# Kernel optimization log

Measured on AMD Instinct MI355X. Metric: run time of the kernel, lower is better.

## Reference

```python
import jax, jax.numpy as jnp
import numpy as np

B, D, HID = 16384, 1024, 4096
HALF = D // 2


def setup_inputs() -> dict:
    key = jax.random.key(0)
    ks = jax.random.split(key, 9)
    sc_in = 1.0 / np.sqrt(HALF)
    sc_h = 1.0 / np.sqrt(HID)
    return {
        "z": jax.random.normal(ks[0], (B, D), dtype=jnp.float32),
        "W1s": jax.random.uniform(ks[1], (HALF, HID), jnp.float32, -sc_in, sc_in),
        "b1s": jax.random.uniform(ks[2], (HID,), jnp.float32, -sc_in, sc_in),
        "W2s": jax.random.uniform(ks[3], (HID, HALF), jnp.float32, -sc_h, sc_h),
        "b2s": jax.random.uniform(ks[4], (HALF,), jnp.float32, -sc_h, sc_h),
        "W1t": jax.random.uniform(ks[5], (HALF, HID), jnp.float32, -sc_in, sc_in),
        "b1t": jax.random.uniform(ks[6], (HID,), jnp.float32, -sc_in, sc_in),
        "W2t": jax.random.uniform(ks[7], (HID, HALF), jnp.float32, -sc_h, sc_h),
        "b2t": jax.random.uniform(ks[8], (HALF,), jnp.float32, -sc_h, sc_h),
    }


def reference(z, W1s, b1s, W2s, b2s, W1t, b1t, W2t, b2t):
    # mask_even=True: a = even-indexed features, b = odd-indexed features
    a = z[:, 0::2]  # [B, HALF]
    b = z[:, 1::2]  # [B, HALF]
    # two-layer MLPs for s and t (cond=None -> inp = a)
    s = jnp.maximum(a @ W1s + b1s, 0.0) @ W2s + b2s  # [B, HALF]
    t = jnp.maximum(a @ W1t + b1t, 0.0) @ W2t + b2t  # [B, HALF]
    b_out = b * jnp.exp(s) + t
    logdet = s.sum(axis=1)  # [B]
    # scatter back: a -> even slots, b_out -> odd slots (interleave)
    z_out = jnp.stack([a, b_out], axis=-1).reshape(z.shape)
    return z_out, logdet
```

## Files before the change

### kernel.cpp

```cpp
#include <hip/hip_runtime.h>
#include <hip/hip_bf16.h>
#include <cstdint>
#include <cstddef>

#define BROWS  16384
#define DDIM   1024
#define HID_N  4096
#define HALF_K 512
#define LDH    8192

typedef __attribute__((ext_vector_type(8))) short s8v;
typedef __attribute__((ext_vector_type(4))) float f4v;

__device__ __forceinline__ void gload16(const void* g, void* l) {
  __builtin_amdgcn_global_load_lds(
      (const __attribute__((address_space(1))) unsigned int*)g,
      (__attribute__((address_space(3))) unsigned int*)l, 16, 0, 0);
}
#define BAR()   asm volatile("s_barrier" ::: "memory")
#define BARS()  asm volatile("s_waitcnt lgkmcnt(0)\n\ts_barrier" ::: "memory")
#define SCHED0() __builtin_amdgcn_sched_barrier(0)

template <int N> __device__ __forceinline__ void vmw() {
  if constexpr (N == 0)      asm volatile("s_waitcnt vmcnt(0)" ::: "memory");
  else if constexpr (N == 4) asm volatile("s_waitcnt vmcnt(4)" ::: "memory");
  else if constexpr (N == 8) asm volatile("s_waitcnt vmcnt(8)" ::: "memory");
}

__global__ __launch_bounds__(256) void cast_a_kernel(const float* __restrict__ z,
                                                     __hip_bfloat16* __restrict__ a16) {
  const int idx = blockIdx.x * 256 + threadIdx.x;
  const int m  = idx >> 6;
  const int kb = idx & 63;
  const float4* zp = (const float4*)(z + (size_t)m * DDIM + (size_t)kb * 16);
  alignas(16) __hip_bfloat16 t[8];
#pragma unroll
  for (int i = 0; i < 4; ++i) {
    float4 v = zp[i];
    t[2 * i]     = __float2bfloat16(v.x);
    t[2 * i + 1] = __float2bfloat16(v.z);
  }
  *(s8v*)(a16 + (size_t)m * HALF_K + kb * 8) = *(const s8v*)t;
}

__global__ __launch_bounds__(256) void transpose_cast_kernel(const float* __restrict__ W,
                                                             __hip_bfloat16* __restrict__ WT,
                                                             int K, int N) {
  __shared__ float tile[32][33];
  const int n0 = blockIdx.x * 32, k0 = blockIdx.y * 32;
  const int tx = threadIdx.x & 31;
  const int ty = threadIdx.x >> 5;
#pragma unroll
  for (int i = 0; i < 32; i += 8)
    tile[ty + i][tx] = W[(size_t)(k0 + ty + i) * N + n0 + tx];
  __syncthreads();
#pragma unroll
  for (int i = 0; i < 32; i += 8)
    WT[(size_t)(n0 + ty + i) * K + k0 + tx] = __float2bfloat16(tile[tx][ty + i]);
}

__global__ __launch_bounds__(512, 2)
void gemm1_kernel(const __hip_bfloat16* __restrict__ A,
                  const __hip_bfloat16* __restrict__ BT,
                  const float* __restrict__ b1s, const float* __restrict__ b1t,
                  __hip_bfloat16* __restrict__ Hout) {
  __shared__ alignas(16) char smem[131072];
  constexpr int NT = HALF_K / 64;

  const int nwg = gridDim.x;
  const int orig = blockIdx.x;
  const int vid = (orig & 7) * (nwg >> 3) + (orig >> 3);
  const int bx = vid >> 5, by = vid & 31;
  const int m0 = bx * 256, n0 = by * 256;

  const int tid = threadIdx.x;
  const int trow = tid >> 3;
  const int scol = ((tid & 7) * 16) ^ ((trow & 7) << 4);

  const int lane = tid & 63, wid = tid >> 6;
  const int wr = wid >> 2, wc = wid & 3;
  const int lr = lane & 15, lk = lane >> 4;
  const int xo = (lr & 7) << 4;

  int aoff[4][2], boff[2][2];
#pragma unroll
  for (int j = 0; j < 4; ++j)
#pragma unroll
    for (int kk = 0; kk < 2; ++kk)
      aoff[j][kk] = (j * 32 + wr * 16 + lr) * 128 + ((kk * 64 + lk * 16) ^ xo);
#pragma unroll
  for (int nn = 0; nn < 2; ++nn)
#pragma unroll
    for (int kk = 0; kk < 2; ++kk)
      boff[nn][kk] = (nn * 64 + wc * 16 + lr) * 128 + ((kk * 64 + lk * 16) ^ xo);

  f4v acc[8][4] = {};

  auto stage_A = [&](int h, int T) {
#pragma unroll
    for (int l = 0; l < 2; ++l)
      gload16((const char*)A + (size_t)(m0 + h * 128 + l * 64 + trow) * (HALF_K * 2) + (size_t)T * 128 + scol,
              smem + (T & 1) * 65536 + h * 16384 + l * 8192 + tid * 16);
  };
  auto stage_B = [&](int h, int T) {
#pragma unroll
    for (int l = 0; l < 2; ++l)
      gload16((const char*)BT + (size_t)(n0 + h * 128 + l * 64 + trow) * (HALF_K * 2) + (size_t)T * 128 + scol,
              smem + (T & 1) * 65536 + 32768 + h * 16384 + l * 8192 + tid * 16);
  };

  stage_A(0, 0); stage_B(0, 0); stage_A(1, 0); stage_B(1, 0);
  stage_A(0, 1); stage_B(0, 1);
  vmw<4>();
  BAR();

  for (int T = 0; T < NT; ++T) {
    const char* bufp = smem + (T & 1) * 65536;
    s8v af[4][2], b0r[2][2], b1r[2][2];

#pragma unroll
    for (int j = 0; j < 4; ++j) {
      af[j][0] = *(const s8v*)(bufp + aoff[j][0]);
      af[j][1] = *(const s8v*)(bufp + aoff[j][1]);
    }
#pragma unroll
    for (int nn = 0; nn < 2; ++nn) {
      b0r[nn][0] = *(const s8v*)(bufp + 32768 + boff[nn][0]);
      b0r[nn][1] = *(const s8v*)(bufp + 32768 + boff[nn][1]);
    }
    if (T + 1 < NT) stage_B(1, T + 1);
    BAR(); SCHED0();
    __builtin_amdgcn_s_setprio(1);
#pragma unroll
    for (int j = 0; j < 4; ++j)
#pragma unroll
      for (int nn = 0; nn < 2; ++nn)
#pragma unroll
        for (int kk = 0; kk < 2; ++kk)
          acc[j][nn] = __builtin_amdgcn_mfma_f32_16x16x32_bf16(af[j][kk], b0r[nn][kk], acc[j][nn], 0, 0, 0);
    __builtin_amdgcn_s_setprio(0);
    BAR();

#pragma unroll
    for (int nn = 0; nn < 2; ++nn) {
      b1r[nn][0] = *(const s8v*)(bufp + 49152 + boff[nn][0]);
      b1r[nn][1] = *(const s8v*)(bufp + 49152 + boff[nn][1]);
    }
    if (T + 1 < NT) stage_A(1, T + 1);
    BAR(); SCHED0();
    __builtin_amdgcn_s_setprio(1);
#pragma unroll
    for (int j = 0; j < 4; ++j)
#pragma unroll
      for (int nn = 0; nn < 2; ++nn)
#pragma unroll
        for (int kk = 0; kk < 2; ++kk)
          acc[j][2 + nn] = __builtin_amdgcn_mfma_f32_16x16x32_bf16(af[j][kk], b1r[nn][kk], acc[j][2 + nn], 0, 0, 0);
    __builtin_amdgcn_s_setprio(0);
    BAR();

#pragma unroll
    for (int j = 0; j < 4; ++j) {
      af[j][0] = *(const s8v*)(bufp + 16384 + aoff[j][0]);
      af[j][1] = *(const s8v*)(bufp + 16384 + aoff[j][1]);
    }
    if (T + 2 < NT) stage_A(0, T + 2);
    BAR(); SCHED0();
    __builtin_amdgcn_s_setprio(1);
#pragma unroll
    for (int j = 0; j < 4; ++j)
#pragma unroll
      for (int nn = 0; nn < 2; ++nn)
#pragma unroll
        for (int kk = 0; kk < 2; ++kk)
          acc[4 + j][nn] = __builtin_amdgcn_mfma_f32_16x16x32_bf16(af[j][kk], b0r[nn][kk], acc[4 + j][nn], 0, 0, 0);
    __builtin_amdgcn_s_setprio(0);
    BAR();

    if (T + 2 < NT) stage_B(0, T + 2);
    SCHED0();
    __builtin_amdgcn_s_setprio(1);
#pragma unroll
    for (int j = 0; j < 4; ++j)
#pragma unroll
      for (int nn = 0; nn < 2; ++nn)
#pragma unroll
        for (int kk = 0; kk < 2; ++kk)
          acc[4 + j][2 + nn] = __builtin_amdgcn_mfma_f32_16x16x32_bf16(af[j][kk], b1r[nn][kk], acc[4 + j][2 + nn], 0, 0, 0);
    __builtin_amdgcn_s_setprio(0);
    if (T + 2 >= NT) vmw<0>(); else vmw<4>();
    BAR();
  }

  const float* bp = (n0 < HID_N) ? b1s : b1t;
  const int cb0 = n0 & (HID_N - 1);
  float bv[4];
#pragma unroll
  for (int ni = 0; ni < 4; ++ni) bv[ni] = bp[cb0 + ni * 64 + wc * 16 + lr];
  const int rbase = wr * 16 + lk * 4;

#pragma unroll
  for (int mi = 0; mi < 8; ++mi) {
    BARS();
#pragma unroll
    for (int ni = 0; ni < 4; ++ni) {
      const int cb = (ni * 64 + wc * 16 + lr) * 2;
#pragma unroll
      for (int r = 0; r < 4; ++r) {
        const int row = rbase + r;
        float v = fmaxf(acc[mi][ni][r] + bv[ni], 0.0f);
        *(__hip_bfloat16*)(smem + row * 512 + (cb ^ ((row & 7) << 4))) = __float2bfloat16(v);
      }
    }
    BARS();
#pragma unroll
    for (int i = 0; i < 2; ++i) {
      const int bo = tid * 32 + i * 16;
      const int row = bo >> 9, cb = bo & 511;
      s8v v = *(const s8v*)(smem + row * 512 + (cb ^ ((row & 7) << 4)));
      *(s8v*)((char*)Hout + ((size_t)(m0 + mi * 32 + row) * LDH + n0) * 2 + cb) = v;
    }
  }
}

__global__ __launch_bounds__(512, 2)
void gemm2_kernel(const __hip_bfloat16* __restrict__ H,
                  const __hip_bfloat16* __restrict__ BsT,
                  const __hip_bfloat16* __restrict__ BtT,
                  const float* __restrict__ b2s, const float* __restrict__ b2t,
                  const float* __restrict__ zin, float* __restrict__ zout,
                  float* __restrict__ gpart) {
  __shared__ alignas(16) char smem[131072];
  constexpr int NT = HID_N / 64;

  const int nwg = gridDim.x;
  const int orig = blockIdx.x;
  const int vid = (orig & 7) * (nwg >> 3) + (orig >> 3);
  const int rb = vid >> 2, by = vid & 3;
  const int m0 = rb * 128, n0c = by * 128;

  const int tid = threadIdx.x;
  const int trow = tid >> 3;
  const int scol = ((tid & 7) * 16) ^ ((trow & 7) << 4);

  const int lane = tid & 63, wid = tid >> 6;
  const int wr = wid >> 2, wc = wid & 3;
  const int lr = lane & 15, lk = lane >> 4;
  const int xo = (lr & 7) << 4;

  int aoff[4][2], boff[2][2];
#pragma unroll
  for (int j = 0; j < 4; ++j)
#pragma unroll
    for (int kk = 0; kk < 2; ++kk)
      aoff[j][kk] = (j * 32 + wr * 16 + lr) * 128 + ((kk * 64 + lk * 16) ^ xo);
#pragma unroll
  for (int nn = 0; nn < 2; ++nn)
#pragma unroll
    for (int kk = 0; kk < 2; ++kk)
      boff[nn][kk] = (nn * 64 + wc * 16 + lr) * 128 + ((kk * 64 + lk * 16) ^ xo);

  f4v as[4][2] = {}, at[4][2] = {};

  auto stage_As = [&](int T) {
#pragma unroll
    for (int l = 0; l < 2; ++l)
      gload16((const char*)H + (size_t)(m0 + l * 64 + trow) * (LDH * 2) + (size_t)T * 128 + scol,
              smem + (T & 1) * 65536 + l * 8192 + tid * 16);
  };
  auto stage_At = [&](int T) {
#pragma unroll
    for (int l = 0; l < 2; ++l)
      gload16((const char*)H + (size_t)(m0 + l * 64 + trow) * (LDH * 2) + 8192 + (size_t)T * 128 + scol,
              smem + (T & 1) * 65536 + 16384 + l * 8192 + tid * 16);
  };
  auto stage_Bs = [&](int T) {
#pragma unroll
    for (int l = 0; l < 2; ++l)
      gload16((const char*)BsT + (size_t)(n0c + l * 64 + trow) * (HID_N * 2) + (size_t)T * 128 + scol,
              smem + (T & 1) * 65536 + 32768 + l * 8192 + tid * 16);
  };
  auto stage_Bt = [&](int T) {
#pragma unroll
    for (int l = 0; l < 2; ++l)
      gload16((const char*)BtT + (size_t)(n0c + l * 64 + trow) * (HID_N * 2) + (size_t)T * 128 + scol,
              smem + (T & 1) * 65536 + 49152 + l * 8192 + tid * 16);
  };

  stage_As(0); stage_Bs(0); stage_At(0); stage_Bt(0); stage_As(1); stage_Bs(1);
  vmw<8>();
  BAR();

  for (int T = 0; T < NT; ++T) {
    const char* bufp = smem + (T & 1) * 65536;
    s8v af[4][2], bfr[2][2];

#pragma unroll
    for (int j = 0; j < 4; ++j) {
      af[j][0] = *(const s8v*)(bufp + aoff[j][0]);
      af[j][1] = *(const s8v*)(bufp + aoff[j][1]);
    }
#pragma unroll
    for (int nn = 0; nn < 2; ++nn) {
      bfr[nn][0] = *(const s8v*)(bufp + 32768 + boff[nn][0]);
      bfr[nn][1] = *(const s8v*)(bufp + 32768 + boff[nn][1]);
    }
    if (T + 1 < NT) { stage_At(T + 1); stage_Bt(T + 1); }
    BAR(); SCHED0();
    __builtin_amdgcn_s_setprio(1);
#pragma unroll
    for (int j = 0; j < 4; ++j)
#pragma unroll
      for (int nn = 0; nn < 2; ++nn)
#pragma unroll
        for (int kk = 0; kk < 2; ++kk)
          as[j][nn] = __builtin_amdgcn_mfma_f32_16x16x32_bf16(af[j][kk], bfr[nn][kk], as[j][nn], 0, 0, 0);
    __builtin_amdgcn_s_setprio(0);
    if (T + 1 >= NT) vmw<0>(); else vmw<8>();
    BAR();

#pragma unroll
    for (int j = 0; j < 4; ++j) {
      af[j][0] = *(const s8v*)(bufp + 16384 + aoff[j][0]);
      af[j][1] = *(const s8v*)(bufp + 16384 + aoff[j][1]);
    }
#pragma unroll
    for (int nn = 0; nn < 2; ++nn) {
      bfr[nn][0] = *(const s8v*)(bufp + 49152 + boff[nn][0]);
      bfr[nn][1] = *(const s8v*)(bufp + 49152 + boff[nn][1]);
    }
    if (T + 2 < NT) { stage_As(T + 2); stage_Bs(T + 2); }
    BAR(); SCHED0();
    __builtin_amdgcn_s_setprio(1);
#pragma unroll
    for (int j = 0; j < 4; ++j)
#pragma unroll
      for (int nn = 0; nn < 2; ++nn)
#pragma unroll
        for (int kk = 0; kk < 2; ++kk)
          at[j][nn] = __builtin_amdgcn_mfma_f32_16x16x32_bf16(af[j][kk], bfr[nn][kk], at[j][nn], 0, 0, 0);
    __builtin_amdgcn_s_setprio(0);
    if (T + 2 >= NT) vmw<0>(); else vmw<8>();
    BAR();
  }

  float bvs[2], bvt[2];
#pragma unroll
  for (int ni = 0; ni < 2; ++ni) {
    const int c = n0c + ni * 64 + wc * 16 + lr;
    bvs[ni] = b2s[c];
    bvt[ni] = b2t[c];
  }
  float pl[4][4] = {};
#pragma unroll
  for (int mi = 0; mi < 4; ++mi) {
#pragma unroll
    for (int ni = 0; ni < 2; ++ni) {
      const int cg = n0c + ni * 64 + wc * 16 + lr;
#pragma unroll
      for (int r = 0; r < 4; ++r) {
        const int rr = m0 + mi * 32 + wr * 16 + lk * 4 + r;
        const float sv = as[mi][ni][r] + bvs[ni];
        const float tv = at[mi][ni][r] + bvt[ni];
        pl[mi][r] += sv;
        const size_t base = (size_t)rr * DDIM + 2 * cg;
        float2 zv = *(const float2*)(zin + base);
        float2 o;
        o.x = zv.x;
        o.y = zv.y * __expf(sv) + tv;
        *(float2*)(zout + base) = o;
      }
    }
  }
#pragma unroll
  for (int m = 1; m < 16; m <<= 1)
#pragma unroll
    for (int mi = 0; mi < 4; ++mi)
#pragma unroll
      for (int r = 0; r < 4; ++r)
        pl[mi][r] += __shfl_xor(pl[mi][r], m, 64);

  float (*ldp)[4] = (float (*)[4])smem;
  BARS();
  if (lr == 0) {
#pragma unroll
    for (int mi = 0; mi < 4; ++mi)
#pragma unroll
      for (int r = 0; r < 4; ++r)
        ldp[mi * 32 + wr * 16 + lk * 4 + r][wc] = pl[mi][r];
  }
  BARS();
  if (tid < 128) {
    float v = ldp[tid][0] + ldp[tid][1] + ldp[tid][2] + ldp[tid][3];
    gpart[(size_t)(m0 + tid) * 4 + by] = v;
  }
}

__global__ __launch_bounds__(256) void ld_reduce_kernel(const float* __restrict__ gpart,
                                                        float* __restrict__ ld) {
  const int r = blockIdx.x * 256 + threadIdx.x;
  float4 v = ((const float4*)gpart)[r];
  ld[r] = v.x + v.y + v.z + v.w;
}

extern "C" void kernel_launch(void* const* d_in, const int* in_sizes, int n_in,
                              void* d_out, int out_size, void* d_ws, size_t ws_size,
                              hipStream_t stream) {
  const float* z   = (const float*)d_in[0];
  const float* W1s = (const float*)d_in[1];
  const float* b1s = (const float*)d_in[2];
  const float* W2s = (const float*)d_in[3];
  const float* b2s = (const float*)d_in[4];
  const float* W1t = (const float*)d_in[5];
  const float* b1t = (const float*)d_in[6];
  const float* W2t = (const float*)d_in[7];
  const float* b2t = (const float*)d_in[8];
  float* zout = (float*)d_out;
  float* ld   = zout + (size_t)BROWS * DDIM;

  char* ws = (char*)d_ws;
  __hip_bfloat16* a16    = (__hip_bfloat16*)ws;
  __hip_bfloat16* w1catT = (__hip_bfloat16*)(ws + 16777216);
  __hip_bfloat16* w2sT   = (__hip_bfloat16*)(ws + 25165824);
  __hip_bfloat16* w2tT   = (__hip_bfloat16*)(ws + 29360128);
  float*          gpart  = (float*)(ws + 33554432);
  char*           hbase  = ws + 33816576;

  int CH = 2048;
  for (int c = 8192; c >= 2048; c >>= 1) {
    if (33816576ull + (size_t)c * 16384ull <= ws_size) { CH = c; break; }
  }
  __hip_bfloat16* H = (__hip_bfloat16*)hbase;

  cast_a_kernel<<<BROWS * (HALF_K / 8) / 256, 256, 0, stream>>>(z, a16);
  transpose_cast_kernel<<<dim3(128, 16), 256, 0, stream>>>(W1s, w1catT, HALF_K, HID_N);
  transpose_cast_kernel<<<dim3(128, 16), 256, 0, stream>>>(W1t, w1catT + (size_t)HID_N * HALF_K, HALF_K, HID_N);
  transpose_cast_kernel<<<dim3(16, 128), 256, 0, stream>>>(W2s, w2sT, HID_N, HALF_K);
  transpose_cast_kernel<<<dim3(16, 128), 256, 0, stream>>>(W2t, w2tT, HID_N, HALF_K);

  for (int mb = 0; mb < BROWS; mb += CH) {
    gemm1_kernel<<<(CH / 256) * 32, 512, 0, stream>>>(
        a16 + (size_t)mb * HALF_K, w1catT, b1s, b1t, H);
    gemm2_kernel<<<(CH / 128) * 4, 512, 0, stream>>>(
        H, w2sT, w2tT, b2s, b2t,
        z + (size_t)mb * DDIM, zout + (size_t)mb * DDIM, gpart + (size_t)mb * 4);
  }
  ld_reduce_kernel<<<BROWS / 256, 256, 0, stream>>>(gpart, ld);
}
```

Measured before the change: 370.4 us.

## Retile second GEMM to 256-row blocks with K=32 steps and batch H epilogue stores

The second GEMM now uses a 256x128 output tile per workgroup with 32-wide K steps and a 4x4 MFMA fragment grid per wave. This raises arithmetic intensity and cuts the LDS footprint, at the cost of twice as many K iterations and barriers. The first GEMM's epilogue now writes the whole tile to LDS before one barrier and then issues nontemporal vectorised stores, with an extra swizzle bit to avoid bank conflicts. The logdet partials are written directly per wave (8 per row) without the LDS reduction, the chunk size doubles, and the output stores are marked nontemporal.

```diff
diff --git a/kernel.cpp b/kernel.cpp
--- a/kernel.cpp
+++ b/kernel.cpp
@@ -11,6 +11,7 @@
 
 typedef __attribute__((ext_vector_type(8))) short s8v;
 typedef __attribute__((ext_vector_type(4))) float f4v;
+typedef __attribute__((ext_vector_type(2))) float f2v;
 
 __device__ __forceinline__ void gload16(const void* g, void* l) {
   __builtin_amdgcn_global_load_lds(
@@ -24,7 +25,7 @@
 template <int N> __device__ __forceinline__ void vmw() {
   if constexpr (N == 0)      asm volatile("s_waitcnt vmcnt(0)" ::: "memory");
   else if constexpr (N == 4) asm volatile("s_waitcnt vmcnt(4)" ::: "memory");
-  else if constexpr (N == 8) asm volatile("s_waitcnt vmcnt(8)" ::: "memory");
+  else if constexpr (N == 6) asm volatile("s_waitcnt vmcnt(6)" ::: "memory");
 }
 
 __global__ __launch_bounds__(256) void cast_a_kernel(const float* __restrict__ z,
@@ -197,29 +198,30 @@
   float bv[4];
 #pragma unroll
   for (int ni = 0; ni < 4; ++ni) bv[ni] = bp[cb0 + ni * 64 + wc * 16 + lr];
-  const int rbase = wr * 16 + lk * 4;
 
 #pragma unroll
   for (int mi = 0; mi < 8; ++mi) {
-    BARS();
 #pragma unroll
     for (int ni = 0; ni < 4; ++ni) {
       const int cb = (ni * 64 + wc * 16 + lr) * 2;
 #pragma unroll
       for (int r = 0; r < 4; ++r) {
-        const int row = rbase + r;
+        const int row = mi * 32 + wr * 16 + lk * 4 + r;
+        const int swz = ((row & 7) << 4) ^ (((row >> 3) & 1) << 8);
         float v = fmaxf(acc[mi][ni][r] + bv[ni], 0.0f);
-        *(__hip_bfloat16*)(smem + row * 512 + (cb ^ ((row & 7) << 4))) = __float2bfloat16(v);
+        *(__hip_bfloat16*)(smem + row * 512 + (cb ^ swz)) = __float2bfloat16(v);
       }
     }
-    BARS();
-#pragma unroll
-    for (int i = 0; i < 2; ++i) {
-      const int bo = tid * 32 + i * 16;
-      const int row = bo >> 9, cb = bo & 511;
-      s8v v = *(const s8v*)(smem + row * 512 + (cb ^ ((row & 7) << 4)));
-      *(s8v*)((char*)Hout + ((size_t)(m0 + mi * 32 + row) * LDH + n0) * 2 + cb) = v;
-    }
+  }
+  BARS();
+#pragma unroll
+  for (int i = 0; i < 16; ++i) {
+    const int bo = tid * 16 + i * 8192;
+    const int row = bo >> 9, cb = bo & 511;
+    const int swz = ((row & 7) << 4) ^ (((row >> 3) & 1) << 8);
+    s8v v = *(const s8v*)(smem + row * 512 + (cb ^ swz));
+    __builtin_nontemporal_store(v,
+        (s8v*)((char*)Hout + ((size_t)(m0 + row) * LDH + n0) * 2 + cb));
   }
 }
 
@@ -230,177 +232,148 @@
                   const float* __restrict__ b2s, const float* __restrict__ b2t,
                   const float* __restrict__ zin, float* __restrict__ zout,
                   float* __restrict__ gpart) {
-  __shared__ alignas(16) char smem[131072];
-  constexpr int NT = HID_N / 64;
+  __shared__ alignas(16) char smem[98304];
+  constexpr int NT = HID_N / 32;
 
   const int nwg = gridDim.x;
   const int orig = blockIdx.x;
-  const int vid = (orig & 7) * (nwg >> 3) + (orig >> 3);
+  const int vid = ((nwg & 7) == 0) ? (orig & 7) * (nwg >> 3) + (orig >> 3) : orig;
   const int rb = vid >> 2, by = vid & 3;
-  const int m0 = rb * 128, n0c = by * 128;
+  const int m0 = rb * 256, n0c = by * 128;
 
   const int tid = threadIdx.x;
-  const int trow = tid >> 3;
-  const int scol = ((tid & 7) * 16) ^ ((trow & 7) << 4);
+  const int trow = tid >> 2;
+  const int scol = (((tid & 3) ^ ((tid >> 3) & 3)) << 4);
 
   const int lane = tid & 63, wid = tid >> 6;
-  const int wr = wid >> 2, wc = wid & 3;
+  const int wm = wid >> 1, wn = wid & 1;
   const int lr = lane & 15, lk = lane >> 4;
-  const int xo = (lr & 7) << 4;
-
-  int aoff[4][2], boff[2][2];
-#pragma unroll
-  for (int j = 0; j < 4; ++j)
-#pragma unroll
-    for (int kk = 0; kk < 2; ++kk)
-      aoff[j][kk] = (j * 32 + wr * 16 + lr) * 128 + ((kk * 64 + lk * 16) ^ xo);
-#pragma unroll
-  for (int nn = 0; nn < 2; ++nn)
-#pragma unroll
-    for (int kk = 0; kk < 2; ++kk)
-      boff[nn][kk] = (nn * 64 + wc * 16 + lr) * 128 + ((kk * 64 + lk * 16) ^ xo);
-
-  f4v as[4][2] = {}, at[4][2] = {};
+
+  int aoff[4], boff[4];
+#pragma unroll
+  for (int f = 0; f < 4; ++f) {
+    const int ra = f * 64 + wm * 16 + lr;
+    aoff[f] = ra * 64 + ((lk * 16) ^ (((ra >> 1) & 3) << 4));
+    const int rbx = f * 32 + wn * 16 + lr;
+    boff[f] = rbx * 64 + ((lk * 16) ^ (((rbx >> 1) & 3) << 4));
+  }
+
+  f4v as[4][4] = {}, at4[4][4] = {};
 
   auto stage_As = [&](int T) {
 #pragma unroll
     for (int l = 0; l < 2; ++l)
-      gload16((const char*)H + (size_t)(m0 + l * 64 + trow) * (LDH * 2) + (size_t)T * 128 + scol,
-              smem + (T & 1) * 65536 + l * 8192 + tid * 16);
+      gload16((const char*)H + (size_t)(m0 + l * 128 + trow) * (LDH * 2) + (size_t)T * 64 + scol,
+              smem + (T & 1) * 49152 + l * 8192 + tid * 16);
   };
   auto stage_At = [&](int T) {
 #pragma unroll
     for (int l = 0; l < 2; ++l)
-      gload16((const char*)H + (size_t)(m0 + l * 64 + trow) * (LDH * 2) + 8192 + (size_t)T * 128 + scol,
-              smem + (T & 1) * 65536 + 16384 + l * 8192 + tid * 16);
+      gload16((const char*)H + (size_t)(m0 + l * 128 + trow) * (LDH * 2) + 8192 + (size_t)T * 64 + scol,
+              smem + (T & 1) * 49152 + 16384 + l * 8192 + tid * 16);
   };
   auto stage_Bs = [&](int T) {
-#pragma unroll
-    for (int l = 0; l < 2; ++l)
-      gload16((const char*)BsT + (size_t)(n0c + l * 64 + trow) * (HID_N * 2) + (size_t)T * 128 + scol,
-              smem + (T & 1) * 65536 + 32768 + l * 8192 + tid * 16);
+    gload16((const char*)BsT + (size_t)(n0c + trow) * (HID_N * 2) + (size_t)T * 64 + scol,
+            smem + (T & 1) * 49152 + 32768 + tid * 16);
   };
   auto stage_Bt = [&](int T) {
-#pragma unroll
-    for (int l = 0; l < 2; ++l)
-      gload16((const char*)BtT + (size_t)(n0c + l * 64 + trow) * (HID_N * 2) + (size_t)T * 128 + scol,
-              smem + (T & 1) * 65536 + 49152 + l * 8192 + tid * 16);
+    gload16((const char*)BtT + (size_t)(n0c + trow) * (HID_N * 2) + (size_t)T * 64 + scol,
+            smem + (T & 1) * 49152 + 40960 + tid * 16);
   };
 
   stage_As(0); stage_Bs(0); stage_At(0); stage_Bt(0); stage_As(1); stage_Bs(1);
-  vmw<8>();
+  vmw<6>();
   BAR();
 
   for (int T = 0; T < NT; ++T) {
-    const char* bufp = smem + (T & 1) * 65536;
-    s8v af[4][2], bfr[2][2];
-
-#pragma unroll
-    for (int j = 0; j < 4; ++j) {
-      af[j][0] = *(const s8v*)(bufp + aoff[j][0]);
-      af[j][1] = *(const s8v*)(bufp + aoff[j][1]);
-    }
-#pragma unroll
-    for (int nn = 0; nn < 2; ++nn) {
-      bfr[nn][0] = *(const s8v*)(bufp + 32768 + boff[nn][0]);
-      bfr[nn][1] = *(const s8v*)(bufp + 32768 + boff[nn][1]);
-    }
+    const char* bufp = smem + (T & 1) * 49152;
+    s8v af[4], bfr[4];
+
+#pragma unroll
+    for (int f = 0; f < 4; ++f) af[f] = *(const s8v*)(bufp + aoff[f]);
+#pragma unroll
+    for (int f = 0; f < 4; ++f) bfr[f] = *(const s8v*)(bufp + 32768 + boff[f]);
     if (T + 1 < NT) { stage_At(T + 1); stage_Bt(T + 1); }
     BAR(); SCHED0();
     __builtin_amdgcn_s_setprio(1);
 #pragma unroll
-    for (int j = 0; j < 4; ++j)
-#pragma unroll
-      for (int nn = 0; nn < 2; ++nn)
-#pragma unroll
-        for (int kk = 0; kk < 2; ++kk)
-          as[j][nn] = __builtin_amdgcn_mfma_f32_16x16x32_bf16(af[j][kk], bfr[nn][kk], as[j][nn], 0, 0, 0);
-    __builtin_amdgcn_s_setprio(0);
-    if (T + 1 >= NT) vmw<0>(); else vmw<8>();
-    BAR();
-
-#pragma unroll
-    for (int j = 0; j < 4; ++j) {
-      af[j][0] = *(const s8v*)(bufp + 16384 + aoff[j][0]);
-      af[j][1] = *(const s8v*)(bufp + 16384 + aoff[j][1]);
-    }
-#pragma unroll
-    for (int nn = 0; nn < 2; ++nn) {
-      bfr[nn][0] = *(const s8v*)(bufp + 49152 + boff[nn][0]);
-      bfr[nn][1] = *(const s8v*)(bufp + 49152 + boff[nn][1]);
-    }
+    for (int fm = 0; fm < 4; ++fm)
+#pragma unroll
+      for (int fn = 0; fn < 4; ++fn)
+        as[fm][fn] = __builtin_amdgcn_mfma_f32_16x16x32_bf16(af[fm], bfr[fn], as[fm][fn], 0, 0, 0);
+    __builtin_amdgcn_s_setprio(0);
+    if (T + 1 >= NT) vmw<0>(); else vmw<6>();
+    BAR();
+
+#pragma unroll
+    for (int f = 0; f < 4; ++f) af[f] = *(const s8v*)(bufp + 16384 + aoff[f]);
+#pragma unroll
+    for (int f = 0; f < 4; ++f) bfr[f] = *(const s8v*)(bufp + 40960 + boff[f]);
     if (T + 2 < NT) { stage_As(T + 2); stage_Bs(T + 2); }
     BAR(); SCHED0();
     __builtin_amdgcn_s_setprio(1);
 #pragma unroll
-    for (int j = 0; j < 4; ++j)
-#pragma unroll
-      for (int nn = 0; nn < 2; ++nn)
-#pragma unroll
-        for (int kk = 0; kk < 2; ++kk)
-          at[j][nn] = __builtin_amdgcn_mfma_f32_16x16x32_bf16(af[j][kk], bfr[nn][kk], at[j][nn], 0, 0, 0);
-    __builtin_amdgcn_s_setprio(0);
-    if (T + 2 >= NT) vmw<0>(); else vmw<8>();
-    BAR();
-  }
-
-  float bvs[2], bvt[2];
-#pragma unroll
-  for (int ni = 0; ni < 2; ++ni) {
-    const int c = n0c + ni * 64 + wc * 16 + lr;
-    bvs[ni] = b2s[c];
-    bvt[ni] = b2t[c];
+    for (int fm = 0; fm < 4; ++fm)
+#pragma unroll
+      for (int fn = 0; fn < 4; ++fn)
+        at4[fm][fn] = __builtin_amdgcn_mfma_f32_16x16x32_bf16(af[fm], bfr[fn], at4[fm][fn], 0, 0, 0);
+    __builtin_amdgcn_s_setprio(0);
+    if (T + 2 >= NT) vmw<0>(); else vmw<6>();
+    BAR();
+  }
+
+  float bvs[4], bvt[4];
+#pragma unroll
+  for (int fn = 0; fn < 4; ++fn) {
+    const int c = n0c + fn * 32 + wn * 16 + lr;
+    bvs[fn] = b2s[c];
+    bvt[fn] = b2t[c];
   }
   float pl[4][4] = {};
 #pragma unroll
-  for (int mi = 0; mi < 4; ++mi) {
-#pragma unroll
-    for (int ni = 0; ni < 2; ++ni) {
-      const int cg = n0c + ni * 64 + wc * 16 + lr;
+  for (int fm = 0; fm < 4; ++fm) {
+#pragma unroll
+    for (int fn = 0; fn < 4; ++fn) {
+      const int cg = n0c + fn * 32 + wn * 16 + lr;
 #pragma unroll
       for (int r = 0; r < 4; ++r) {
-        const int rr = m0 + mi * 32 + wr * 16 + lk * 4 + r;
-        const float sv = as[mi][ni][r] + bvs[ni];
-        const float tv = at[mi][ni][r] + bvt[ni];
-        pl[mi][r] += sv;
+        const int rr = m0 + fm * 64 + wm * 16 + lk * 4 + r;
+        const float sv = as[fm][fn][r] + bvs[fn];
+        const float tv = at4[fm][fn][r] + bvt[fn];
+        pl[fm][r] += sv;
         const size_t base = (size_t)rr * DDIM + 2 * cg;
         float2 zv = *(const float2*)(zin + base);
-        float2 o;
+        f2v o;
         o.x = zv.x;
         o.y = zv.y * __expf(sv) + tv;
-        *(float2*)(zout + base) = o;
+        __builtin_nontemporal_store(o, (f2v*)(zout + base));
       }
     }
   }
 #pragma unroll
   for (int m = 1; m < 16; m <<= 1)
 #pragma unroll
-    for (int mi = 0; mi < 4; ++mi)
+    for (int fm = 0; fm < 4; ++fm)
 #pragma unroll
       for (int r = 0; r < 4; ++r)
-        pl[mi][r] += __shfl_xor(pl[mi][r], m, 64);
-
-  float (*ldp)[4] = (float (*)[4])smem;
-  BARS();
+        pl[fm][r] += __shfl_xor(pl[fm][r], m, 64);
   if (lr == 0) {
 #pragma unroll
-    for (int mi = 0; mi < 4; ++mi)
-#pragma unroll
-      for (int r = 0; r < 4; ++r)
-        ldp[mi * 32 + wr * 16 + lk * 4 + r][wc] = pl[mi][r];
-  }
-  BARS();
-  if (tid < 128) {
-    float v = ldp[tid][0] + ldp[tid][1] + ldp[tid][2] + ldp[tid][3];
-    gpart[(size_t)(m0 + tid) * 4 + by] = v;
+    for (int fm = 0; fm < 4; ++fm)
+#pragma unroll
+      for (int r = 0; r < 4; ++r) {
+        const int rr = m0 + fm * 64 + wm * 16 + lk * 4 + r;
+        gpart[(size_t)rr * 8 + by * 2 + wn] = pl[fm][r];
+      }
   }
 }
 
 __global__ __launch_bounds__(256) void ld_reduce_kernel(const float* __restrict__ gpart,
                                                         float* __restrict__ ld) {
   const int r = blockIdx.x * 256 + threadIdx.x;
-  float4 v = ((const float4*)gpart)[r];
-  ld[r] = v.x + v.y + v.z + v.w;
+  const float4* g = (const float4*)(gpart + (size_t)r * 8);
+  float4 v0 = g[0], v1 = g[1];
+  ld[r] = ((v0.x + v0.y) + (v0.z + v0.w)) + ((v1.x + v1.y) + (v1.z + v1.w));
 }
 
 extern "C" void kernel_launch(void* const* d_in, const int* in_sizes, int n_in,
@@ -424,11 +397,11 @@
   __hip_bfloat16* w2sT   = (__hip_bfloat16*)(ws + 25165824);
   __hip_bfloat16* w2tT   = (__hip_bfloat16*)(ws + 29360128);
   float*          gpart  = (float*)(ws + 33554432);
-  char*           hbase  = ws + 33816576;
-
-  int CH = 2048;
-  for (int c = 8192; c >= 2048; c >>= 1) {
-    if (33816576ull + (size_t)c * 16384ull <= ws_size) { CH = c; break; }
+  char*           hbase  = ws + 34078720;
+
+  int CH = 4096;
+  for (int c = 16384; c >= 4096; c >>= 1) {
+    if (34078720ull + (size_t)c * 16384ull <= ws_size) { CH = c; break; }
   }
   __hip_bfloat16* H = (__hip_bfloat16*)hbase;
 
@@ -441,9 +414,9 @@
   for (int mb = 0; mb < BROWS; mb += CH) {
     gemm1_kernel<<<(CH / 256) * 32, 512, 0, stream>>>(
         a16 + (size_t)mb * HALF_K, w1catT, b1s, b1t, H);
-    gemm2_kernel<<<(CH / 128) * 4, 512, 0, stream>>>(
+    gemm2_kernel<<<(CH / 256) * 4, 512, 0, stream>>>(
         H, w2sT, w2tT, b2s, b2t,
-        z + (size_t)mb * DDIM, zout + (size_t)mb * DDIM, gpart + (size_t)mb * 4);
+        z + (size_t)mb * DDIM, zout + (size_t)mb * DDIM, gpart + (size_t)mb * 8);
   }
   ld_reduce_kernel<<<BROWS / 256, 256, 0, stream>>>(gpart, ld);
 }
```

Result: slower. 535.4 us (+44.5%).
